# Kernel optimization log

Measured on AMD Instinct MI355X. Metric: run time of the kernel, lower is better.

The kernel has to match this reference:

```python
import jax, jax.numpy as jnp
import numpy as np

BINS = jnp.array([1, 2, 3, 4, 8, 16, 32, 64], dtype=jnp.int32)
L = 10      # max span width
HID = 150   # Score hidden dim


def _mlp(x, W1, b1, W2, b2, W3, b3):
    # Score module: Linear -> ReLU -> Linear -> ReLU -> Linear (dropout = identity at eval)
    h = jax.nn.relu(x @ W1 + b1)
    h = jax.nn.relu(h @ W2 + b2)
    return h @ W3 + b3


def setup_inputs() -> dict:
    key = jax.random.key(0)
    ks = jax.random.split(key, 16)
    T, A, E, D, S = 8192, 1024, 512, 20, 32768
    GI = 2 * A + E + D  # 2580
    sc = lambda n: 1.0 / np.sqrt(n)
    return {
        "states": jax.random.normal(ks[0], (T, A), jnp.float32),
        "embeds": jax.random.normal(ks[1], (T, E), jnp.float32),
        "span_starts": jnp.sort(jax.random.randint(ks[2], (S,), 0, T - L)),
        "span_lengths": jax.random.randint(ks[3], (S,), 0, L),
        # attention Score params (attn_dim -> 150 -> 150 -> 1)
        "Wa1": jax.random.normal(ks[4], (A, HID), jnp.float32) * sc(A),
        "ba1": jnp.zeros((HID,), jnp.float32),
        "Wa2": jax.random.normal(ks[5], (HID, HID), jnp.float32) * sc(HID),
        "ba2": jnp.zeros((HID,), jnp.float32),
        "Wa3": jax.random.normal(ks[6], (HID, 1), jnp.float32) * sc(HID),
        "ba3": jnp.zeros((1,), jnp.float32),
        # Distance embedding table (len(bins)+1 = 9 buckets)
        "width_table": jax.random.normal(ks[7], (9, D), jnp.float32) * 0.1,
        # mention Score params (gi_dim -> 150 -> 150 -> 1)
        "Ws1": jax.random.normal(ks[8], (GI, HID), jnp.float32) * sc(GI),
        "bs1": jnp.zeros((HID,), jnp.float32),
        "Ws2": jax.random.normal(ks[9], (HID, HID), jnp.float32) * sc(HID),
        "bs2": jnp.zeros((HID,), jnp.float32),
        "Ws3": jax.random.normal(ks[10], (HID, 1), jnp.float32) * sc(HID),
        "bs3": jnp.zeros((1,), jnp.float32),
    }


def reference(states, embeds, span_starts, span_lengths,
              Wa1, ba1, Wa2, ba2, Wa3, ba3,
              width_table,
              Ws1, bs1, Ws2, bs2, Ws3, bs3):
    T = states.shape[0]
    # per-token attention logits: [T, 1]
    attns = _mlp(states, Wa1, ba1, Wa2, ba2, Wa3, ba3)

    pos = jnp.arange(L)
    idx = span_starts[:, None] + pos[None, :]                 # [S, L]
    mask = pos[None, :] <= span_lengths[:, None]              # valid positions
    idx = jnp.minimum(idx, T - 1)

    span_attn = jnp.where(mask, attns[idx, 0], -jnp.inf)      # [S, L]
    w = jax.nn.softmax(span_attn, axis=1)                     # per-span softmax
    pooled = jnp.einsum('sl,sle->se', w, embeds[idx])         # [S, E]

    ends = span_starts + span_lengths
    widths = span_lengths + 1
    bucket = jnp.searchsorted(BINS, widths.astype(jnp.int32), side='right')
    size_emb = width_table[bucket]                            # [S, D]

    g = jnp.concatenate([states[span_starts], states[ends], pooled, size_emb], axis=-1)
    scores = _mlp(g, Ws1, bs1, Ws2, bs2, Ws3, bs3)[:, 0]      # [S]
    return scores
```

## Files before the change

### kernel.cpp

```cpp
#include <hip/hip_runtime.h>
#include <math.h>

#define T_TOK 8192
#define A_DIM 1024
#define E_DIM 512
#define S_SPAN 32768
#define HID 150

typedef __attribute__((ext_vector_type(8))) short short8;
typedef __attribute__((ext_vector_type(4))) float f32x4;
typedef __attribute__((ext_vector_type(4))) unsigned int u32x4;
typedef __attribute__((ext_vector_type(4))) unsigned short u16x4;

__device__ __forceinline__ unsigned short f2bf(float f) {
    unsigned int u = __builtin_bit_cast(unsigned int, f);
    u += 0x7FFFu + ((u >> 16) & 1u);
    return (unsigned short)(u >> 16);
}

#define NS4 (T_TOK * A_DIM / 4)
#define NE4 (T_TOK * E_DIM / 4)
#define NCAST ((NS4 + NE4 + 255) / 256)

struct WConv { const float* src; unsigned short* dst; int K0; int Kpad; int nblk; };
struct PrepTab {
    const float* s; const float* e; unsigned short* sd; unsigned short* ed;
    WConv g[6];
    const float* wt; const float* Ws1w; float* PW;
};

__global__ __launch_bounds__(256) void prep_kernel(PrepTab tab) {
    int b = blockIdx.x;
    if (b < NCAST) {
        int idx = b * 256 + threadIdx.x;
        const float* src; unsigned short* dst;
        if (idx < NS4) { src = tab.s; dst = tab.sd; }
        else { idx -= NS4; if (idx >= NE4) return; src = tab.e; dst = tab.ed; }
        f32x4 v = *(const f32x4*)(src + (size_t)idx * 4);
        u16x4 o;
        o.x = f2bf(v.x); o.y = f2bf(v.y); o.z = f2bf(v.z); o.w = f2bf(v.w);
        *(u16x4*)(dst + (size_t)idx * 4) = o;
        return;
    }
    b -= NCAST;
    #pragma unroll
    for (int gi = 0; gi < 6; ++gi) {
        if (b < tab.g[gi].nblk) {
            int idx = b * 256 + threadIdx.x;
            int Kpad = tab.g[gi].Kpad;
            if (idx < Kpad * 160) {
                int k = idx / 160, j = idx - k * 160;
                float v = (j < HID && k < tab.g[gi].K0)
                          ? tab.g[gi].src[(size_t)k * HID + j] : 0.f;
                tab.g[gi].dst[(size_t)j * Kpad + k] = f2bf(v);
            }
            return;
        }
        b -= tab.g[gi].nblk;
    }
    int j = threadIdx.x;
    if (j < HID) {
        float acc = 0.f;
        for (int k = 0; k < 20; ++k)
            acc = fmaf(tab.wt[b * 20 + k], tab.Ws1w[k * HID + j], acc);
        tab.PW[b * HID + j] = acc;
    }
}

struct GG {
    const unsigned short* A; int lda;
    const unsigned short* W; int K; int nrb;
    float* outf; unsigned short* outh; int ldo;
    const float* bias; int relu;
    const float* dotv; const float* dotb; float* dotout;
};
struct GTab { GG g[4]; int ng; };

__global__ __launch_bounds__(256) void gemm_fused(GTab tab) {
    constexpr int LDW = 88;
    __shared__ unsigned short WtL[2][160 * LDW];

    int b = blockIdx.x;
    int gi = 0;
    while (gi < tab.ng - 1 && b >= tab.g[gi].nrb) { b -= tab.g[gi].nrb; ++gi; }
    const GG G = tab.g[gi];

    const int tid = threadIdx.x;
    const int wid = tid >> 6;
    const int lane = tid & 63;
    const int l15 = lane & 15;
    const int quad = lane >> 4;
    const int row0 = b * 64 + wid * 16 + l15;
    const int K = G.K;
    const int nch = K >> 6;
    const unsigned short* Arow = G.A + (size_t)row0 * G.lda;

    u32x4 stg[5];
    int sn[5], sk[5];
    #pragma unroll
    for (int i = 0; i < 5; ++i) { int u = tid + i * 256; sn[i] = u >> 3; sk[i] = (u & 7) * 8; }

    f32x4 acc[10];
    #pragma unroll
    for (int nt = 0; nt < 10; ++nt) acc[nt] = (f32x4){0.f, 0.f, 0.f, 0.f};

    #pragma unroll
    for (int i = 0; i < 5; ++i)
        stg[i] = *(const u32x4*)(G.W + (size_t)sn[i] * K + sk[i]);
    short8 avc0 = *(const short8*)(Arow + quad * 8);
    short8 avc1 = *(const short8*)(Arow + 32 + quad * 8);
    #pragma unroll
    for (int i = 0; i < 5; ++i)
        *(u32x4*)&WtL[0][sn[i] * LDW + sk[i]] = stg[i];
    __syncthreads();

    for (int c = 0; c < nch; ++c) {
        const int pb = c & 1;
        short8 avn0, avn1;
        const bool more = (c + 1 < nch);
        if (more) {
            const int kn = (c + 1) << 6;
            #pragma unroll
            for (int i = 0; i < 5; ++i)
                stg[i] = *(const u32x4*)(G.W + (size_t)sn[i] * K + kn + sk[i]);
            avn0 = *(const short8*)(Arow + kn + quad * 8);
            avn1 = *(const short8*)(Arow + kn + 32 + quad * 8);
        }
        #pragma unroll
        for (int nt = 0; nt < 10; ++nt) {
            short8 bv0 = *(const short8*)&WtL[pb][(nt * 16 + l15) * LDW + quad * 8];
            acc[nt] = __builtin_amdgcn_mfma_f32_16x16x32_bf16(avc0, bv0, acc[nt], 0, 0, 0);
            short8 bv1 = *(const short8*)&WtL[pb][(nt * 16 + l15) * LDW + 32 + quad * 8];
            acc[nt] = __builtin_amdgcn_mfma_f32_16x16x32_bf16(avc1, bv1, acc[nt], 0, 0, 0);
        }
        if (more) {
            #pragma unroll
            for (int i = 0; i < 5; ++i)
                *(u32x4*)&WtL[pb ^ 1][sn[i] * LDW + sk[i]] = stg[i];
            avc0 = avn0; avc1 = avn1;
        }
        __syncthreads();
    }

    const int rbase = b * 64 + wid * 16 + quad * 4;
    if (G.dotout) {
        float part[4] = {0.f, 0.f, 0.f, 0.f};
        #pragma unroll
        for (int nt = 0; nt < 10; ++nt) {
            int col = nt * 16 + l15;
            float bv_ = (col < HID) ? G.bias[col] : 0.f;
            float vv = (col < HID) ? G.dotv[col] : 0.f;
            #pragma unroll
            for (int r = 0; r < 4; ++r)
                part[r] += fmaxf(acc[nt][r] + bv_, 0.f) * vv;
        }
        #pragma unroll
        for (int r = 0; r < 4; ++r) {
            float p = part[r];
            #pragma unroll
            for (int off = 1; off < 16; off <<= 1) p += __shfl_xor(p, off);
            if (l15 == 0) G.dotout[rbase + r] = p + G.dotb[0];
        }
    } else {
        #pragma unroll
        for (int nt = 0; nt < 10; ++nt) {
            int col = nt * 16 + l15;
            float bv_ = (G.bias != nullptr && col < HID) ? G.bias[col] : 0.f;
            #pragma unroll
            for (int r = 0; r < 4; ++r) {
                int row = rbase + r;
                float v = acc[nt][r] + bv_;
                if (G.relu) v = fmaxf(v, 0.f);
                if (G.outh) G.outh[(size_t)row * G.ldo + col] = f2bf(v);
                else        G.outf[(size_t)row * G.ldo + col] = v;
            }
        }
    }
}

__global__ __launch_bounds__(256) void span_l1_kernel(const float* __restrict__ attns,
                                                      const int* __restrict__ starts,
                                                      const int* __restrict__ lens,
                                                      const float* __restrict__ Ps,
                                                      const float* __restrict__ Pe,
                                                      const float* __restrict__ Pm,
                                                      const float* __restrict__ PW,
                                                      const float* __restrict__ bs1,
                                                      unsigned short* __restrict__ SH1) {
    const int wid = threadIdx.x >> 6, lane = threadIdx.x & 63;
    const int s = blockIdx.x * 4 + wid;
    const int start = starts[s];
    const int len = lens[s];

    const int iv = min(start + lane, T_TOK - 1);
    float a = (lane <= len) ? attns[iv] : -INFINITY;
    float m = a;
    #pragma unroll
    for (int off = 32; off; off >>= 1) m = fmaxf(m, __shfl_xor(m, off));
    float e = (lane <= len) ? __expf(a - m) : 0.f;
    float ssum = e;
    #pragma unroll
    for (int off = 32; off; off >>= 1) ssum += __shfl_xor(ssum, off);
    float wv = e / ssum;

    float wl[10]; int il[10];
    #pragma unroll
    for (int l = 0; l < 10; ++l) { wl[l] = __shfl(wv, l); il[l] = __shfl(iv, l); }

    const int end = start + len;
    const int width = len + 1;
    const int bucket = (width >= 1) + (width >= 2) + (width >= 3) + (width >= 4) +
                       (width >= 8) + (width >= 16) + (width >= 32) + (width >= 64);

    for (int j = lane; j < HID; j += 64) {
        float acc = bs1[j] + Ps[(size_t)start * 160 + j] + Pe[(size_t)end * 160 + j] +
                    PW[bucket * HID + j];
        #pragma unroll
        for (int l = 0; l < 10; ++l) acc = fmaf(wl[l], Pm[(size_t)il[l] * 160 + j], acc);
        SH1[(size_t)s * 192 + j] = f2bf(fmaxf(acc, 0.f));
    }
}

extern "C" void kernel_launch(void* const* d_in, const int* in_sizes, int n_in,
                              void* d_out, int out_size, void* d_ws, size_t ws_size,
                              hipStream_t stream) {
    const float* states = (const float*)d_in[0];
    const float* embeds = (const float*)d_in[1];
    const int* span_starts = (const int*)d_in[2];
    const int* span_lengths = (const int*)d_in[3];
    const float* Wa1 = (const float*)d_in[4];
    const float* ba1 = (const float*)d_in[5];
    const float* Wa2 = (const float*)d_in[6];
    const float* ba2 = (const float*)d_in[7];
    const float* Wa3 = (const float*)d_in[8];
    const float* ba3 = (const float*)d_in[9];
    const float* width_table = (const float*)d_in[10];
    const float* Ws1 = (const float*)d_in[11];
    const float* bs1 = (const float*)d_in[12];
    const float* Ws2 = (const float*)d_in[13];
    const float* bs2 = (const float*)d_in[14];
    const float* Ws3 = (const float*)d_in[15];
    const float* bs3 = (const float*)d_in[16];
    float* out = (float*)d_out;

    char* w = (char*)d_ws;
    unsigned short* WtA  = (unsigned short*)w;  w += 480 * 1024 * 2;
    unsigned short* WtE  = (unsigned short*)w;  w += 160 * 512 * 2;
    unsigned short* Wa2t = (unsigned short*)w;  w += 160 * 192 * 2;
    unsigned short* Ws2t = (unsigned short*)w;  w += 160 * 192 * 2;
    float* PW    = (float*)w;                   w += 5632;
    float* attns = (float*)w;                   w += 8192 * 4;
    unsigned short* Sbf = (unsigned short*)w;   w += (size_t)T_TOK * A_DIM * 2;
    unsigned short* Ebf = (unsigned short*)w;   w += (size_t)T_TOK * E_DIM * 2;
    float* Ps = (float*)w;                      w += (size_t)T_TOK * 160 * 4;
    float* Pe = (float*)w;                      w += (size_t)T_TOK * 160 * 4;
    float* Pm = (float*)w;                      w += (size_t)T_TOK * 160 * 4;
    unsigned short* H1A = (unsigned short*)w;   w += (size_t)T_TOK * 192 * 2;
    unsigned short* SH1 = (unsigned short*)w;   w += (size_t)S_SPAN * 192 * 2;

    PrepTab pt;
    pt.s = states; pt.e = embeds; pt.sd = Sbf; pt.ed = Ebf;
    pt.g[0] = { Wa1,              WtA,              1024, 1024, (160*1024 + 255)/256 };
    pt.g[1] = { Ws1,              WtA + 160*1024,   1024, 1024, (160*1024 + 255)/256 };
    pt.g[2] = { Ws1 + 1024*150,   WtA + 320*1024,   1024, 1024, (160*1024 + 255)/256 };
    pt.g[3] = { Ws1 + 2048*150,   WtE,               512,  512, (160*512  + 255)/256 };
    pt.g[4] = { Wa2,              Wa2t,              150,  192, (160*192  + 255)/256 };
    pt.g[5] = { Ws2,              Ws2t,              150,  192, (160*192  + 255)/256 };
    pt.wt = width_table; pt.Ws1w = Ws1 + 2560*150; pt.PW = PW;
    int wblk = 0; for (int i = 0; i < 6; ++i) wblk += pt.g[i].nblk;
    prep_kernel<<<NCAST + wblk + 9, 256, 0, stream>>>(pt);

    GG z = {};

    GTab t1; t1.ng = 4;
    t1.g[0] = z; t1.g[0].A = Sbf; t1.g[0].lda = 1024; t1.g[0].W = WtA;            t1.g[0].K = 1024;
    t1.g[0].nrb = 128; t1.g[0].outh = H1A; t1.g[0].ldo = 192; t1.g[0].bias = ba1; t1.g[0].relu = 1;
    t1.g[1] = z; t1.g[1].A = Sbf; t1.g[1].lda = 1024; t1.g[1].W = WtA + 160*1024; t1.g[1].K = 1024;
    t1.g[1].nrb = 128; t1.g[1].outf = Ps;  t1.g[1].ldo = 160;
    t1.g[2] = z; t1.g[2].A = Sbf; t1.g[2].lda = 1024; t1.g[2].W = WtA + 320*1024; t1.g[2].K = 1024;
    t1.g[2].nrb = 128; t1.g[2].outf = Pe;  t1.g[2].ldo = 160;
    t1.g[3] = z; t1.g[3].A = Ebf; t1.g[3].lda = 512;  t1.g[3].W = WtE;            t1.g[3].K = 512;
    t1.g[3].nrb = 128; t1.g[3].outf = Pm;  t1.g[3].ldo = 160;
    gemm_fused<<<512, 256, 0, stream>>>(t1);

    GTab t2; t2.ng = 1;
    t2.g[0] = z; t2.g[0].A = H1A; t2.g[0].lda = 192; t2.g[0].W = Wa2t; t2.g[0].K = 192;
    t2.g[0].nrb = 128; t2.g[0].bias = ba2; t2.g[0].dotv = Wa3; t2.g[0].dotb = ba3; t2.g[0].dotout = attns;
    gemm_fused<<<128, 256, 0, stream>>>(t2);

    span_l1_kernel<<<S_SPAN / 4, 256, 0, stream>>>(attns, span_starts, span_lengths,
                                                   Ps, Pe, Pm, PW, bs1, SH1);

    GTab t3; t3.ng = 1;
    t3.g[0] = z; t3.g[0].A = SH1; t3.g[0].lda = 192; t3.g[0].W = Ws2t; t3.g[0].K = 192;
    t3.g[0].nrb = 512; t3.g[0].bias = bs2; t3.g[0].dotv = Ws3; t3.g[0].dotb = bs3; t3.g[0].dotout = out;
    gemm_fused<<<512, 256, 0, stream>>>(t3);
}
```

Measured before the change: 180.8 us.

## Store token projections as bf16 and tile weight transposes through LDS

The per-token projection outputs Ps, Pe and Pm are now written as bf16 instead of fp32. This halves the gather traffic in the span layer-1 kernel, which reads 12 rows per span, and that kernel now loads two bf16 values per 32-bit access. The weight-transpose prep now goes through a shared-memory tile of 64 rows, so both the global reads and the global writes are coalesced. The cost is lower precision in the intermediate projections. The output-type branch in the GEMM epilogue is also removed.

Result: slower. 191.1 us (+5.7%).

```diff
diff --git a/kernel.cpp b/kernel.cpp
--- a/kernel.cpp
+++ b/kernel.cpp
@@ -17,10 +17,14 @@
     u += 0x7FFFu + ((u >> 16) & 1u);
     return (unsigned short)(u >> 16);
 }
+__device__ __forceinline__ float bf2f(unsigned int h16) {
+    unsigned int u = h16 << 16;
+    return __builtin_bit_cast(float, u);
+}
 
 #define NS4 (T_TOK * A_DIM / 4)
 #define NE4 (T_TOK * E_DIM / 4)
-#define NCAST ((NS4 + NE4 + 255) / 256)
+#define NCAST ((NS4 + NE4) / 256)
 
 struct WConv { const float* src; unsigned short* dst; int K0; int Kpad; int nblk; };
 struct PrepTab {
@@ -30,12 +34,13 @@
 };
 
 __global__ __launch_bounds__(256) void prep_kernel(PrepTab tab) {
+    __shared__ unsigned short tile[64 * 161];
     int b = blockIdx.x;
     if (b < NCAST) {
         int idx = b * 256 + threadIdx.x;
         const float* src; unsigned short* dst;
         if (idx < NS4) { src = tab.s; dst = tab.sd; }
-        else { idx -= NS4; if (idx >= NE4) return; src = tab.e; dst = tab.ed; }
+        else { idx -= NS4; src = tab.e; dst = tab.ed; }
         f32x4 v = *(const f32x4*)(src + (size_t)idx * 4);
         u16x4 o;
         o.x = f2bf(v.x); o.y = f2bf(v.y); o.z = f2bf(v.z); o.w = f2bf(v.w);
@@ -46,13 +51,20 @@
     #pragma unroll
     for (int gi = 0; gi < 6; ++gi) {
         if (b < tab.g[gi].nblk) {
-            int idx = b * 256 + threadIdx.x;
-            int Kpad = tab.g[gi].Kpad;
-            if (idx < Kpad * 160) {
-                int k = idx / 160, j = idx - k * 160;
-                float v = (j < HID && k < tab.g[gi].K0)
-                          ? tab.g[gi].src[(size_t)k * HID + j] : 0.f;
-                tab.g[gi].dst[(size_t)j * Kpad + k] = f2bf(v);
+            const int k0 = b * 64;
+            const int K0 = tab.g[gi].K0, Kpad = tab.g[gi].Kpad;
+            const float* src = tab.g[gi].src;
+            unsigned short* dst = tab.g[gi].dst;
+            for (int idx = threadIdx.x; idx < 64 * 160; idx += 256) {
+                int kr = idx / 160, j = idx - kr * 160;
+                int k = k0 + kr;
+                float v = (j < HID && k < K0) ? src[(size_t)k * HID + j] : 0.f;
+                tile[kr * 161 + j] = f2bf(v);
+            }
+            __syncthreads();
+            for (int idx = threadIdx.x; idx < 160 * 64; idx += 256) {
+                int j = idx >> 6, kc = idx & 63;
+                dst[(size_t)j * Kpad + k0 + kc] = tile[kc * 161 + j];
             }
             return;
         }
@@ -70,7 +82,7 @@
 struct GG {
     const unsigned short* A; int lda;
     const unsigned short* W; int K; int nrb;
-    float* outf; unsigned short* outh; int ldo;
+    unsigned short* outh; int ldo;
     const float* bias; int relu;
     const float* dotv; const float* dotb; float* dotout;
 };
@@ -171,8 +183,7 @@
                 int row = rbase + r;
                 float v = acc[nt][r] + bv_;
                 if (G.relu) v = fmaxf(v, 0.f);
-                if (G.outh) G.outh[(size_t)row * G.ldo + col] = f2bf(v);
-                else        G.outf[(size_t)row * G.ldo + col] = v;
+                G.outh[(size_t)row * G.ldo + col] = f2bf(v);
             }
         }
     }
@@ -181,9 +192,9 @@
 __global__ __launch_bounds__(256) void span_l1_kernel(const float* __restrict__ attns,
                                                       const int* __restrict__ starts,
                                                       const int* __restrict__ lens,
-                                                      const float* __restrict__ Ps,
-                                                      const float* __restrict__ Pe,
-                                                      const float* __restrict__ Pm,
+                                                      const unsigned short* __restrict__ Ps,
+                                                      const unsigned short* __restrict__ Pe,
+                                                      const unsigned short* __restrict__ Pm,
                                                       const float* __restrict__ PW,
                                                       const float* __restrict__ bs1,
                                                       unsigned short* __restrict__ SH1) {
@@ -212,12 +223,25 @@
     const int bucket = (width >= 1) + (width >= 2) + (width >= 3) + (width >= 4) +
                        (width >= 8) + (width >= 16) + (width >= 32) + (width >= 64);
 
-    for (int j = lane; j < HID; j += 64) {
-        float acc = bs1[j] + Ps[(size_t)start * 160 + j] + Pe[(size_t)end * 160 + j] +
-                    PW[bucket * HID + j];
-        #pragma unroll
-        for (int l = 0; l < 10; ++l) acc = fmaf(wl[l], Pm[(size_t)il[l] * 160 + j], acc);
-        SH1[(size_t)s * 192 + j] = f2bf(fmaxf(acc, 0.f));
+    const unsigned short* ps = Ps + (size_t)start * 160;
+    const unsigned short* pe = Pe + (size_t)end * 160;
+    const float* pw = PW + bucket * HID;
+
+    for (int p = lane; p < 75; p += 64) {
+        const int j = 2 * p;
+        unsigned int u0 = *(const unsigned int*)(ps + j);
+        unsigned int u1 = *(const unsigned int*)(pe + j);
+        float a0 = bs1[j]     + bf2f(u0 & 0xffff) + bf2f(u1 & 0xffff) + pw[j];
+        float a1 = bs1[j + 1] + bf2f(u0 >> 16)    + bf2f(u1 >> 16)    + pw[j + 1];
+        #pragma unroll
+        for (int l = 0; l < 10; ++l) {
+            unsigned int um = *(const unsigned int*)(Pm + (size_t)il[l] * 160 + j);
+            a0 = fmaf(wl[l], bf2f(um & 0xffff), a0);
+            a1 = fmaf(wl[l], bf2f(um >> 16), a1);
+        }
+        unsigned int packed = (unsigned int)f2bf(fmaxf(a0, 0.f)) |
+                              ((unsigned int)f2bf(fmaxf(a1, 0.f)) << 16);
+        *(unsigned int*)(SH1 + (size_t)s * 192 + j) = packed;
     }
 }
 
@@ -252,23 +276,22 @@
     float* attns = (float*)w;                   w += 8192 * 4;
     unsigned short* Sbf = (unsigned short*)w;   w += (size_t)T_TOK * A_DIM * 2;
     unsigned short* Ebf = (unsigned short*)w;   w += (size_t)T_TOK * E_DIM * 2;
-    float* Ps = (float*)w;                      w += (size_t)T_TOK * 160 * 4;
-    float* Pe = (float*)w;                      w += (size_t)T_TOK * 160 * 4;
-    float* Pm = (float*)w;                      w += (size_t)T_TOK * 160 * 4;
+    unsigned short* Psh = (unsigned short*)w;   w += (size_t)T_TOK * 160 * 2;
+    unsigned short* Peh = (unsigned short*)w;   w += (size_t)T_TOK * 160 * 2;
+    unsigned short* Pmh = (unsigned short*)w;   w += (size_t)T_TOK * 160 * 2;
     unsigned short* H1A = (unsigned short*)w;   w += (size_t)T_TOK * 192 * 2;
     unsigned short* SH1 = (unsigned short*)w;   w += (size_t)S_SPAN * 192 * 2;
 
     PrepTab pt;
     pt.s = states; pt.e = embeds; pt.sd = Sbf; pt.ed = Ebf;
-    pt.g[0] = { Wa1,              WtA,              1024, 1024, (160*1024 + 255)/256 };
-    pt.g[1] = { Ws1,              WtA + 160*1024,   1024, 1024, (160*1024 + 255)/256 };
-    pt.g[2] = { Ws1 + 1024*150,   WtA + 320*1024,   1024, 1024, (160*1024 + 255)/256 };
-    pt.g[3] = { Ws1 + 2048*150,   WtE,               512,  512, (160*512  + 255)/256 };
-    pt.g[4] = { Wa2,              Wa2t,              150,  192, (160*192  + 255)/256 };
-    pt.g[5] = { Ws2,              Ws2t,              150,  192, (160*192  + 255)/256 };
+    pt.g[0] = { Wa1,              WtA,              1024, 1024, 16 };
+    pt.g[1] = { Ws1,              WtA + 160*1024,   1024, 1024, 16 };
+    pt.g[2] = { Ws1 + 1024*150,   WtA + 320*1024,   1024, 1024, 16 };
+    pt.g[3] = { Ws1 + 2048*150,   WtE,               512,  512,  8 };
+    pt.g[4] = { Wa2,              Wa2t,              150,  192,  3 };
+    pt.g[5] = { Ws2,              Ws2t,              150,  192,  3 };
     pt.wt = width_table; pt.Ws1w = Ws1 + 2560*150; pt.PW = PW;
-    int wblk = 0; for (int i = 0; i < 6; ++i) wblk += pt.g[i].nblk;
-    prep_kernel<<<NCAST + wblk + 9, 256, 0, stream>>>(pt);
+    prep_kernel<<<NCAST + 62 + 9, 256, 0, stream>>>(pt);
 
     GG z = {};
 
@@ -276,11 +299,11 @@
     t1.g[0] = z; t1.g[0].A = Sbf; t1.g[0].lda = 1024; t1.g[0].W = WtA;            t1.g[0].K = 1024;
     t1.g[0].nrb = 128; t1.g[0].outh = H1A; t1.g[0].ldo = 192; t1.g[0].bias = ba1; t1.g[0].relu = 1;
     t1.g[1] = z; t1.g[1].A = Sbf; t1.g[1].lda = 1024; t1.g[1].W = WtA + 160*1024; t1.g[1].K = 1024;
-    t1.g[1].nrb = 128; t1.g[1].outf = Ps;  t1.g[1].ldo = 160;
+    t1.g[1].nrb = 128; t1.g[1].outh = Psh; t1.g[1].ldo = 160;
     t1.g[2] = z; t1.g[2].A = Sbf; t1.g[2].lda = 1024; t1.g[2].W = WtA + 320*1024; t1.g[2].K = 1024;
-    t1.g[2].nrb = 128; t1.g[2].outf = Pe;  t1.g[2].ldo = 160;
+    t1.g[2].nrb = 128; t1.g[2].outh = Peh; t1.g[2].ldo = 160;
     t1.g[3] = z; t1.g[3].A = Ebf; t1.g[3].lda = 512;  t1.g[3].W = WtE;            t1.g[3].K = 512;
-    t1.g[3].nrb = 128; t1.g[3].outf = Pm;  t1.g[3].ldo = 160;
+    t1.g[3].nrb = 128; t1.g[3].outh = Pmh; t1.g[3].ldo = 160;
     gemm_fused<<<512, 256, 0, stream>>>(t1);
 
     GTab t2; t2.ng = 1;
@@ -289,7 +312,7 @@
     gemm_fused<<<128, 256, 0, stream>>>(t2);
 
     span_l1_kernel<<<S_SPAN / 4, 256, 0, stream>>>(attns, span_starts, span_lengths,
-                                                   Ps, Pe, Pm, PW, bs1, SH1);
+                                                   Psh, Peh, Pmh, PW, bs1, SH1);
 
     GTab t3; t3.ng = 1;
     t3.g[0] = z; t3.g[0].A = SH1; t3.g[0].lda = 192; t3.g[0].W = Ws2t; t3.g[0].K = 192;
```
